# Kernel optimization log

Measured on AMD Instinct MI355X. Metric: run time of the kernel, lower is better.

Reference implementation:

```python
import jax, jax.numpy as jnp
import numpy as np

B, T, F, H = 2048, 512, 60, 7  # batch, seq_len, input_size, hidden_size


def setup_inputs() -> dict:
    key = jax.random.key(0)
    ks = jax.random.split(key, 9)
    bound = 1.0 / np.sqrt(H)  # PyTorch LSTM init: U(-1/sqrt(H), 1/sqrt(H))
    u = lambda k, s: jax.random.uniform(k, s, jnp.float32, -bound, bound)
    return {
        "x": jax.random.normal(ks[0], (B, T, F), jnp.float32),
        "Wih0": u(ks[1], (4 * H, F)),
        "Whh0": u(ks[2], (4 * H, H)),
        "bih0": u(ks[3], (4 * H,)),
        "bhh0": u(ks[4], (4 * H,)),
        "Wih1": u(ks[5], (4 * H, H)),
        "Whh1": u(ks[6], (4 * H, H)),
        "bih1": u(ks[7], (4 * H,)),
        "bhh1": u(ks[8], (4 * H,)),
    }


def _cell(xt, h, c, Wih, Whh, b):
    # PyTorch gate order: input, forget, cell(g), output
    gates = xt @ Wih.T + h @ Whh.T + b  # [B, 4H]
    i, f, g, o = jnp.split(gates, 4, axis=-1)
    c_new = jax.nn.sigmoid(f) * c + jax.nn.sigmoid(i) * jnp.tanh(g)
    h_new = jax.nn.sigmoid(o) * jnp.tanh(c_new)
    return h_new, c_new


def reference(x, Wih0, Whh0, bih0, bhh0, Wih1, Whh1, bih1, bhh1):
    b0 = bih0 + bhh0
    b1 = bih1 + bhh1
    batch = x.shape[0]
    hid = Whh0.shape[1]
    z = jnp.zeros((batch, hid), x.dtype)

    def step(carry, xt):
        h0, c0, h1, c1 = carry
        h0, c0 = _cell(xt, h0, c0, Wih0, Whh0, b0)
        h1, c1 = _cell(h0, h1, c1, Wih1, Whh1, b1)
        return (h0, c0, h1, c1), None

    xs = jnp.swapaxes(x, 0, 1)  # [T, B, F] for scan over time
    (h0, c0, h1, c1), _ = jax.lax.scan(step, (z, z, z, z), xs)
    # out[:, -1] of batch_first LSTM == final hidden state of top layer
    return h1
```

## Files before the change

kernel.cpp:

```cpp
#include <hip/hip_runtime.h>


#define B_ 2048
#define T_ 512
#define F_ 60
#define H_ 7
#define G4 28
#define BT_ (B_ * T_)
#define L2E 1.4426950408889634f
#define PD 8

#if __has_builtin(__builtin_amdgcn_exp2f)
#define EXP2(x) __builtin_amdgcn_exp2f(x)
#else
#define EXP2(x) exp2f(x)
#endif

__device__ __forceinline__ float rcpf_(float v) { return __builtin_amdgcn_rcpf(v); }

__device__ __forceinline__ float bcast(float v, int srclane) {
    return __uint_as_float(__builtin_amdgcn_readlane(__float_as_uint(v), srclane));
}

__device__ __forceinline__ float dot7(const float* w, const float* h, float seed) {
    float m01 = fmaf(w[1], h[1], w[0] * h[0]);
    float m23 = fmaf(w[3], h[3], w[2] * h[2]);
    float m45 = fmaf(w[5], h[5], w[4] * h[4]);
    float m6  = fmaf(w[6], h[6], seed);
    return (m01 + m23) + (m45 + m6);
}

__global__ __launch_bounds__(256)
void proj_kernel(const float* __restrict__ x, const float* __restrict__ Wih0,
                 const float* __restrict__ bih0, const float* __restrict__ bhh0,
                 float* __restrict__ A)
{
    __shared__ float wsm[G4 * F_];
    __shared__ float bsm[G4];

    for (int i = threadIdx.x; i < G4 * F_; i += 256) wsm[i] = Wih0[i];
    if (threadIdx.x < G4) bsm[threadIdx.x] = bih0[threadIdx.x] + bhh0[threadIdx.x];
    __syncthreads();

    const int bt = blockIdx.x * 256 + threadIdx.x;

    float xr[F_];
    const float4* __restrict__ xp = (const float4*)(x + (size_t)bt * F_);
    #pragma unroll
    for (int j = 0; j < 15; ++j) {
        float4 q = xp[j];
        xr[4 * j + 0] = q.x; xr[4 * j + 1] = q.y;
        xr[4 * j + 2] = q.z; xr[4 * j + 3] = q.w;
    }

    float4* __restrict__ Ap = (float4*)(A + (size_t)bt * G4);
    #pragma unroll
    for (int rg = 0; rg < 7; ++rg) {
        float s[4];
        #pragma unroll
        for (int q = 0; q < 4; ++q) {
            const int r = rg * 4 + q;
            const float* w = &wsm[r * F_];
            float a0 = bsm[r], a1 = 0.f, a2 = 0.f, a3 = 0.f;
            #pragma unroll
            for (int k = 0; k < F_; k += 4) {
                a0 = fmaf(w[k + 0], xr[k + 0], a0);
                a1 = fmaf(w[k + 1], xr[k + 1], a1);
                a2 = fmaf(w[k + 2], xr[k + 2], a2);
                a3 = fmaf(w[k + 3], xr[k + 3], a3);
            }
            s[q] = (a0 + a1) + (a2 + a3);
        }
        Ap[rg] = make_float4(s[0], s[1], s[2], s[3]);
    }
}

__global__ __launch_bounds__(256)
void rec_kernel(const float* __restrict__ A,
                const float* __restrict__ Whh0,
                const float* __restrict__ Wih1, const float* __restrict__ Whh1,
                const float* __restrict__ bih1, const float* __restrict__ bhh1,
                float* __restrict__ out)
{
    const int tid   = threadIdx.x;
    const int lane  = tid & 63;
    const bool isL1 = lane >= 32;
    const int g     = lane & 31;
    const int r     = (g < G4) ? g : (G4 - 1);
    const int b     = blockIdx.x * 4 + (tid >> 6);

    float wA[H_], wB[H_];
    #pragma unroll
    for (int v = 0; v < H_; ++v) {
        wA[v] = isL1 ? Wih1[r * H_ + v] : Whh0[r * H_ + v];
        wB[v] = isL1 ? Whh1[r * H_ + v] : 0.f;
    }
    const float bias1 = bih1[r] + bhh1[r];

    const bool isT = (r >= 2 * H_ && r < 3 * H_);
    const float KK = isT ? (-2.f * L2E) : (-L2E);
    const float Aa = isT ? 2.f : 1.f;
    const float Ca = isT ? -1.f : 0.f;

    float h0v[H_] = {0, 0, 0, 0, 0, 0, 0};
    float h1v[H_] = {0, 0, 0, 0, 0, 0, 0};
    float c = 0.f, hnew = 0.f;

    const float* __restrict__ pa = A + (size_t)b * T_ * G4 + r;

    float buf[PD];
    #pragma unroll
    for (int i = 0; i < PD; ++i) buf[i] = pa[i * G4];

    for (int tt = 0; tt < T_; tt += PD) {
        #pragma unroll
        for (int s = 0; s < PD; ++s) {
            const int t = tt + s;
            const int tn = (t + PD < T_) ? (t + PD) : (T_ - 1);
            float nb = pa[(size_t)tn * G4];

            float seed = isL1 ? bias1 : buf[s];
            float a = dot7(wA, h0v, seed);
            a = dot7(wB, h1v, a);
            float act = fmaf(Aa, rcpf_(1.f + EXP2(KK * a)), Ca);

            float fg = __shfl(act, lane + 7, 64);
            float gg = __shfl(act, lane + 14, 64);
            float og = __shfl(act, lane + 21, 64);

            float cnew = fmaf(fg, c, act * gg);
            if (t == 0) cnew = isL1 ? 0.f : cnew;
            c = cnew;
            float th = fmaf(2.f, rcpf_(1.f + EXP2(-2.f * L2E * c)), -1.f);
            hnew = og * th;

            #pragma unroll
            for (int v = 0; v < H_; ++v) h0v[v] = bcast(hnew, v);
            #pragma unroll
            for (int v = 0; v < H_; ++v) h1v[v] = bcast(hnew, 32 + v);

            buf[s] = nb;
        }
    }

    {
        float a = dot7(wA, h0v, isL1 ? bias1 : 0.f);
        a = dot7(wB, h1v, a);
        float act = fmaf(Aa, rcpf_(1.f + EXP2(KK * a)), Ca);
        float fg = __shfl(act, lane + 7, 64);
        float gg = __shfl(act, lane + 14, 64);
        float og = __shfl(act, lane + 21, 64);
        c = fmaf(fg, c, act * gg);
        float th = fmaf(2.f, rcpf_(1.f + EXP2(-2.f * L2E * c)), -1.f);
        hnew = og * th;
    }

    if (isL1 && g < H_) out[(size_t)b * H_ + g] = hnew;
}

#define CH 16
#define NCH (T_ / CH)
#define F4 15
#define ROW4 (CH * F4)
#define BPB 4
#define TOT4 (BPB * ROW4)

__device__ __forceinline__ float proj32(const float* pw, const float4* rp, float seed) {
    float s0 = seed, s1 = 0.f, s2 = 0.f, s3 = 0.f;
    #pragma unroll
    for (int j = 0; j < 8; ++j) {
        float4 q = rp[j];
        s0 = fmaf(pw[4 * j + 0], q.x, s0);
        s1 = fmaf(pw[4 * j + 1], q.y, s1);
        s2 = fmaf(pw[4 * j + 2], q.z, s2);
        s3 = fmaf(pw[4 * j + 3], q.w, s3);
    }
    return (s0 + s1) + (s2 + s3);
}

__global__ __launch_bounds__(256, 2)
void lstm2_fallback(const float* __restrict__ x,
                    const float* __restrict__ Wih0, const float* __restrict__ Whh0,
                    const float* __restrict__ bih0, const float* __restrict__ bhh0,
                    const float* __restrict__ Wih1, const float* __restrict__ Whh1,
                    const float* __restrict__ bih1, const float* __restrict__ bhh1,
                    float* __restrict__ out)
{
    __shared__ float4 lds4[2][BPB][ROW4];

    const int tid   = threadIdx.x;
    const int lane  = tid & 63;
    const bool isL1 = lane >= 32;
    const int g     = lane & 31;
    const int r     = (g < G4) ? g : (G4 - 1);
    const int grp   = tid >> 6;
    const int b     = blockIdx.x * BPB + grp;

    float pw[32];
    {
        const int offs = isL1 ? 28 : 0;
        #pragma unroll
        for (int k = 0; k < 32; ++k) pw[k] = Wih0[r * F_ + offs + k];
        if (isL1) { pw[0] = pw[1] = pw[2] = pw[3] = 0.f; }
    }
    float wA[H_], wB[H_];
    #pragma unroll
    for (int v = 0; v < H_; ++v) {
        wA[v] = isL1 ? Wih1[r * H_ + v] : Whh0[r * H_ + v];
        wB[v] = isL1 ? Whh1[r * H_ + v] : 0.f;
    }
    const float bias0 = bih0[r] + bhh0[r];
    const float bias1 = bih1[r] + bhh1[r];

    const bool isT = (r >= 2 * H_ && r < 3 * H_);
    const float KK = isT ? (-2.f * L2E) : (-L2E);
    const float Aa = isT ? 2.f : 1.f;
    const float Ca = isT ? -1.f : 0.f;

    float h0v[H_] = {0, 0, 0, 0, 0, 0, 0};
    float h1v[H_] = {0, 0, 0, 0, 0, 0, 0};
    float c = 0.f, hnew = 0.f;

    const float4* __restrict__ xb =
        (const float4*)(x + (size_t)(blockIdx.x * BPB) * T_ * F_);
    const int XB4 = T_ * F4;
    const int lofs = isL1 ? 7 : 0;
    const float pseed = isL1 ? 0.f : bias0;

    #pragma unroll
    for (int i = 0; i < 4; ++i) {
        int idx = tid + 256 * i;
        if (idx < TOT4) {
            int bl = idx / ROW4;
            int j  = idx - bl * ROW4;
            lds4[0][bl][j] = xb[bl * XB4 + j];
        }
    }
    __syncthreads();

    float a_in;
    {
        float ow = proj32(pw, &lds4[0][grp][0] + lofs, pseed);
        a_in = ow + __shfl(ow, lane ^ 32, 64);
    }

    for (int ch = 0; ch < NCH; ++ch) {
        const int cn = (ch < NCH - 1) ? ch + 1 : ch;
        float4 st[4];
        #pragma unroll
        for (int i = 0; i < 4; ++i) {
            int idx = tid + 256 * i;
            if (idx < TOT4) {
                int bl = idx / ROW4;
                int j  = idx - bl * ROW4;
                st[i] = xb[bl * XB4 + cn * ROW4 + j];
            }
        }

        const int buf = ch & 1;
        const float4* __restrict__ rowb = &lds4[buf][grp][0] + lofs;

        #pragma unroll
        for (int s = 0; s < CH; ++s) {
            float seed = isL1 ? bias1 : a_in;
            float a = dot7(wA, h0v, seed);
            a = dot7(wB, h1v, a);
            float act = fmaf(Aa, rcpf_(1.f + EXP2(KK * a)), Ca);

            float fg = __shfl(act, lane + 7, 64);
            float gg = __shfl(act, lane + 14, 64);
            float og = __shfl(act, lane + 21, 64);

            float cnew = fmaf(fg, c, act * gg);
            if (ch == 0 && s == 0) cnew = isL1 ? 0.f : cnew;
            c = cnew;
            float th = fmaf(2.f, rcpf_(1.f + EXP2(-2.f * L2E * c)), -1.f);
            hnew = og * th;

            #pragma unroll
            for (int v = 0; v < H_; ++v) h0v[v] = bcast(hnew, v);
            if (ch > 0 || s > 0) {
                #pragma unroll
                for (int v = 0; v < H_; ++v) h1v[v] = bcast(hnew, 32 + v);
            }

            if (s < CH - 1) {
                float ow = proj32(pw, rowb + (s + 1) * F4, pseed);
                a_in = ow + __shfl(ow, lane ^ 32, 64);
            }
        }

        #pragma unroll
        for (int i = 0; i < 4; ++i) {
            int idx = tid + 256 * i;
            if (idx < TOT4) {
                int bl = idx / ROW4;
                int j  = idx - bl * ROW4;
                lds4[buf ^ 1][bl][j] = st[i];
            }
        }
        __syncthreads();

        if (ch < NCH - 1) {
            float ow = proj32(pw, &lds4[buf ^ 1][grp][0] + lofs, pseed);
            a_in = ow + __shfl(ow, lane ^ 32, 64);
        }
    }

    {
        float a = dot7(wA, h0v, isL1 ? bias1 : 0.f);
        a = dot7(wB, h1v, a);
        float act = fmaf(Aa, rcpf_(1.f + EXP2(KK * a)), Ca);
        float fg = __shfl(act, lane + 7, 64);
        float gg = __shfl(act, lane + 14, 64);
        float og = __shfl(act, lane + 21, 64);
        c = fmaf(fg, c, act * gg);
        float th = fmaf(2.f, rcpf_(1.f + EXP2(-2.f * L2E * c)), -1.f);
        hnew = og * th;
    }

    if (isL1 && g < H_) out[(size_t)b * H_ + g] = hnew;
}

extern "C" void kernel_launch(void* const* d_in, const int* in_sizes, int n_in,
                              void* d_out, int out_size, void* d_ws, size_t ws_size,
                              hipStream_t stream) {
    const float* x    = (const float*)d_in[0];
    const float* Wih0 = (const float*)d_in[1];
    const float* Whh0 = (const float*)d_in[2];
    const float* bih0 = (const float*)d_in[3];
    const float* bhh0 = (const float*)d_in[4];
    const float* Wih1 = (const float*)d_in[5];
    const float* Whh1 = (const float*)d_in[6];
    const float* bih1 = (const float*)d_in[7];
    const float* bhh1 = (const float*)d_in[8];
    float* out = (float*)d_out;

    const size_t need = (size_t)BT_ * G4 * sizeof(float);
    if (ws_size >= need) {
        float* A = (float*)d_ws;
        proj_kernel<<<dim3(BT_ / 256), dim3(256), 0, stream>>>(x, Wih0, bih0, bhh0, A);
        rec_kernel<<<dim3(B_ / 4), dim3(256), 0, stream>>>(A, Whh0, Wih1, Whh1,
                                                           bih1, bhh1, out);
    } else {
        lstm2_fallback<<<dim3(B_ / BPB), dim3(256), 0, stream>>>(
            x, Wih0, Whh0, bih0, bhh0, Wih1, Whh1, bih1, bhh1, out);
    }
}
```

Before: 537.5 us.

## Remap input projection so each lane owns one gate row in registers

The projection kernel now keeps one gate row of Wih0 in registers per lane, and each half-wave processes one timestep row of x. The x loads are uniform across the 32 lanes of a half-wave, so they broadcast, and the output write is coalesced per row. This drops the shared-memory weight staging and the 60-element per-thread x register array. In exchange each lane recomputes nothing but loads 60 weights per thread, and 4 of every 32 lanes are idle, wasting a fraction of compute.

New measurement: 721.7 us. +34.3%, slower.

```diff
diff --git a/kernel.cpp b/kernel.cpp
--- a/kernel.cpp
+++ b/kernel.cpp
@@ -9,6 +9,7 @@
 #define BT_ (B_ * T_)
 #define L2E 1.4426950408889634f
 #define PD 8
+#define RPB 128
 
 #if __has_builtin(__builtin_amdgcn_exp2f)
 #define EXP2(x) __builtin_amdgcn_exp2f(x)
@@ -35,43 +36,38 @@
                  const float* __restrict__ bih0, const float* __restrict__ bhh0,
                  float* __restrict__ A)
 {
-    __shared__ float wsm[G4 * F_];
-    __shared__ float bsm[G4];
-
-    for (int i = threadIdx.x; i < G4 * F_; i += 256) wsm[i] = Wih0[i];
-    if (threadIdx.x < G4) bsm[threadIdx.x] = bih0[threadIdx.x] + bhh0[threadIdx.x];
-    __syncthreads();
-
-    const int bt = blockIdx.x * 256 + threadIdx.x;
-
-    float xr[F_];
-    const float4* __restrict__ xp = (const float4*)(x + (size_t)bt * F_);
-    #pragma unroll
-    for (int j = 0; j < 15; ++j) {
-        float4 q = xp[j];
-        xr[4 * j + 0] = q.x; xr[4 * j + 1] = q.y;
-        xr[4 * j + 2] = q.z; xr[4 * j + 3] = q.w;
-    }
-
-    float4* __restrict__ Ap = (float4*)(A + (size_t)bt * G4);
-    #pragma unroll
-    for (int rg = 0; rg < 7; ++rg) {
-        float s[4];
-        #pragma unroll
-        for (int q = 0; q < 4; ++q) {
-            const int r = rg * 4 + q;
-            const float* w = &wsm[r * F_];
-            float a0 = bsm[r], a1 = 0.f, a2 = 0.f, a3 = 0.f;
-            #pragma unroll
-            for (int k = 0; k < F_; k += 4) {
-                a0 = fmaf(w[k + 0], xr[k + 0], a0);
-                a1 = fmaf(w[k + 1], xr[k + 1], a1);
-                a2 = fmaf(w[k + 2], xr[k + 2], a2);
-                a3 = fmaf(w[k + 3], xr[k + 3], a3);
-            }
-            s[q] = (a0 + a1) + (a2 + a3);
-        }
-        Ap[rg] = make_float4(s[0], s[1], s[2], s[3]);
+    const int lane = threadIdx.x & 63;
+    const int wv   = threadIdx.x >> 6;
+    const int g    = lane & 31;
+    const int r    = (g < G4) ? g : (G4 - 1);
+    const int half = lane >> 5;
+
+    float wg[F_];
+    #pragma unroll
+    for (int k = 0; k < F_; ++k) wg[k] = Wih0[r * F_ + k];
+    const float bias = bih0[r] + bhh0[r];
+
+    const int row0 = blockIdx.x * RPB + wv * 32 + half;
+
+    #pragma unroll 4
+    for (int p = 0; p < 16; ++p) {
+        const int row = row0 + 2 * p;
+        const float4* __restrict__ xp = (const float4*)(x + (size_t)row * F_);
+        float4 q[15];
+        #pragma unroll
+        for (int j = 0; j < 15; ++j) q[j] = xp[j];
+
+        float s0 = bias, s1 = 0.f, s2 = 0.f, s3 = 0.f;
+        #pragma unroll
+        for (int j = 0; j < 15; ++j) {
+            s0 = fmaf(wg[4 * j + 0], q[j].x, s0);
+            s1 = fmaf(wg[4 * j + 1], q[j].y, s1);
+            s2 = fmaf(wg[4 * j + 2], q[j].z, s2);
+            s3 = fmaf(wg[4 * j + 3], q[j].w, s3);
+        }
+        float a = (s0 + s1) + (s2 + s3);
+
+        if (g < G4) A[(size_t)row * G4 + r] = a;
     }
 }
 
@@ -339,7 +335,7 @@
     const size_t need = (size_t)BT_ * G4 * sizeof(float);
     if (ws_size >= need) {
         float* A = (float*)d_ws;
-        proj_kernel<<<dim3(BT_ / 256), dim3(256), 0, stream>>>(x, Wih0, bih0, bhh0, A);
+        proj_kernel<<<dim3(BT_ / RPB), dim3(256), 0, stream>>>(x, Wih0, bih0, bhh0, A);
         rec_kernel<<<dim3(B_ / 4), dim3(256), 0, stream>>>(A, Whh0, Wih1, Whh1,
                                                            bih1, bhh1, out);
     } else {
```

## Interleave gate layout for DPP quad broadcasts and register-tile input projection

Applied to the files above, without the earlier changes.

The input projection kernel now has each thread compute four rows, with weights read as float4 from shared memory and the next x chunk prefetched. Each weight load is then reused across four rows. The A buffer is written in a gate-interleaved order (i,f,g,o adjacent per hidden unit). This lets the recurrent kernel gather gates with DPP quad_perm moves instead of ds_bpermute shuffles, shortening the serial per-step critical path. The recurrent prefetch is restructured into a block load of the next 8 steps. The trade-offs are higher register pressure in the projection kernel (112 accumulators) and more complex indexing.

After: 668.5 us. 24.4% more time.

```diff
diff --git a/kernel.cpp b/kernel.cpp
--- a/kernel.cpp
+++ b/kernel.cpp
@@ -9,12 +9,17 @@
 #define BT_ (B_ * T_)
 #define L2E 1.4426950408889634f
 #define PD 8
+#define RPT 4
+#define PRB (256 * RPT)
 
 #if __has_builtin(__builtin_amdgcn_exp2f)
 #define EXP2(x) __builtin_amdgcn_exp2f(x)
 #else
 #define EXP2(x) exp2f(x)
 #endif
+
+#define QUADB(v, pat) \
+    __int_as_float(__builtin_amdgcn_mov_dpp(__float_as_int(v), pat, 0xF, 0xF, true))
 
 __device__ __forceinline__ float rcpf_(float v) { return __builtin_amdgcn_rcpf(v); }
 
@@ -35,43 +40,63 @@
                  const float* __restrict__ bih0, const float* __restrict__ bhh0,
                  float* __restrict__ A)
 {
-    __shared__ float wsm[G4 * F_];
-    __shared__ float bsm[G4];
-
-    for (int i = threadIdx.x; i < G4 * F_; i += 256) wsm[i] = Wih0[i];
-    if (threadIdx.x < G4) bsm[threadIdx.x] = bih0[threadIdx.x] + bhh0[threadIdx.x];
+    __shared__ float4 wsm4[G4 * 15];
+    __shared__ float  bsm[G4];
+
+    const int tid = threadIdx.x;
+    for (int i = tid; i < G4 * 15; i += 256) wsm4[i] = ((const float4*)Wih0)[i];
+    if (tid < G4) bsm[tid] = bih0[tid] + bhh0[tid];
     __syncthreads();
 
-    const int bt = blockIdx.x * 256 + threadIdx.x;
-
-    float xr[F_];
-    const float4* __restrict__ xp = (const float4*)(x + (size_t)bt * F_);
-    #pragma unroll
+    const int row0 = blockIdx.x * PRB + tid;
+
+    float acc[G4][RPT];
+    #pragma unroll
+    for (int p = 0; p < G4; ++p) {
+        const int r = (p & 3) * 7 + (p >> 2);
+        const float bb = bsm[r];
+        #pragma unroll
+        for (int rr = 0; rr < RPT; ++rr) acc[p][rr] = bb;
+    }
+
+    const float* bp[RPT];
+    #pragma unroll
+    for (int rr = 0; rr < RPT; ++rr) bp[rr] = x + (size_t)(row0 + 256 * rr) * F_;
+
+    float4 qc[RPT], qn[RPT];
+    #pragma unroll
+    for (int rr = 0; rr < RPT; ++rr) qc[rr] = *(const float4*)(bp[rr]);
+
+    #pragma unroll 1
     for (int j = 0; j < 15; ++j) {
-        float4 q = xp[j];
-        xr[4 * j + 0] = q.x; xr[4 * j + 1] = q.y;
-        xr[4 * j + 2] = q.z; xr[4 * j + 3] = q.w;
-    }
-
-    float4* __restrict__ Ap = (float4*)(A + (size_t)bt * G4);
-    #pragma unroll
-    for (int rg = 0; rg < 7; ++rg) {
-        float s[4];
-        #pragma unroll
-        for (int q = 0; q < 4; ++q) {
-            const int r = rg * 4 + q;
-            const float* w = &wsm[r * F_];
-            float a0 = bsm[r], a1 = 0.f, a2 = 0.f, a3 = 0.f;
-            #pragma unroll
-            for (int k = 0; k < F_; k += 4) {
-                a0 = fmaf(w[k + 0], xr[k + 0], a0);
-                a1 = fmaf(w[k + 1], xr[k + 1], a1);
-                a2 = fmaf(w[k + 2], xr[k + 2], a2);
-                a3 = fmaf(w[k + 3], xr[k + 3], a3);
-            }
-            s[q] = (a0 + a1) + (a2 + a3);
-        }
-        Ap[rg] = make_float4(s[0], s[1], s[2], s[3]);
+        const int jn = (j < 14) ? j + 1 : 14;
+        #pragma unroll
+        for (int rr = 0; rr < RPT; ++rr)
+            qn[rr] = *(const float4*)(bp[rr] + 4 * jn);
+
+        #pragma unroll
+        for (int p = 0; p < G4; ++p) {
+            const int r = (p & 3) * 7 + (p >> 2);
+            float4 w = wsm4[r * 15 + j];
+            #pragma unroll
+            for (int rr = 0; rr < RPT; ++rr) {
+                acc[p][rr] = fmaf(w.x, qc[rr].x, acc[p][rr]);
+                acc[p][rr] = fmaf(w.y, qc[rr].y, acc[p][rr]);
+                acc[p][rr] = fmaf(w.z, qc[rr].z, acc[p][rr]);
+                acc[p][rr] = fmaf(w.w, qc[rr].w, acc[p][rr]);
+            }
+        }
+        #pragma unroll
+        for (int rr = 0; rr < RPT; ++rr) qc[rr] = qn[rr];
+    }
+
+    #pragma unroll
+    for (int rr = 0; rr < RPT; ++rr) {
+        float4* __restrict__ Ap = (float4*)(A + (size_t)(row0 + 256 * rr) * G4);
+        #pragma unroll
+        for (int u = 0; u < 7; ++u)
+            Ap[u] = make_float4(acc[4 * u + 0][rr], acc[4 * u + 1][rr],
+                                acc[4 * u + 2][rr], acc[4 * u + 3][rr]);
     }
 }
 
@@ -82,12 +107,15 @@
                 const float* __restrict__ bih1, const float* __restrict__ bhh1,
                 float* __restrict__ out)
 {
-    const int tid   = threadIdx.x;
-    const int lane  = tid & 63;
+    const int tid  = threadIdx.x;
+    const int lane = tid & 63;
     const bool isL1 = lane >= 32;
-    const int g     = lane & 31;
-    const int r     = (g < G4) ? g : (G4 - 1);
-    const int b     = blockIdx.x * 4 + (tid >> 6);
+    const int l5 = lane & 31;
+    const int gi = lane & 3;
+    const int u  = l5 >> 2;
+    const int r  = min(gi * 7 + u, G4 - 1);
+    const int pos = min(l5, G4 - 1);
+    const int b  = blockIdx.x * 4 + (tid >> 6);
 
     float wA[H_], wB[H_];
     #pragma unroll
@@ -97,7 +125,7 @@
     }
     const float bias1 = bih1[r] + bhh1[r];
 
-    const bool isT = (r >= 2 * H_ && r < 3 * H_);
+    const bool isT = (gi == 2);
     const float KK = isT ? (-2.f * L2E) : (-L2E);
     const float Aa = isT ? 2.f : 1.f;
     const float Ca = isT ? -1.f : 0.f;
@@ -106,40 +134,45 @@
     float h1v[H_] = {0, 0, 0, 0, 0, 0, 0};
     float c = 0.f, hnew = 0.f;
 
-    const float* __restrict__ pa = A + (size_t)b * T_ * G4 + r;
-
-    float buf[PD];
-    #pragma unroll
-    for (int i = 0; i < PD; ++i) buf[i] = pa[i * G4];
-
+    const float* __restrict__ pa = A + (size_t)b * T_ * G4 + pos;
+
+    float buf[PD], nxt[PD];
+    #pragma unroll
+    for (int i = 0; i < PD; ++i) buf[i] = pa[(size_t)i * G4];
+
+    #pragma unroll 1
     for (int tt = 0; tt < T_; tt += PD) {
+        const bool more = (tt + PD < T_);
+        if (more) {
+            #pragma unroll
+            for (int i = 0; i < PD; ++i) nxt[i] = pa[(size_t)(tt + PD + i) * G4];
+        }
         #pragma unroll
         for (int s = 0; s < PD; ++s) {
-            const int t = tt + s;
-            const int tn = (t + PD < T_) ? (t + PD) : (T_ - 1);
-            float nb = pa[(size_t)tn * G4];
-
             float seed = isL1 ? bias1 : buf[s];
             float a = dot7(wA, h0v, seed);
             a = dot7(wB, h1v, a);
             float act = fmaf(Aa, rcpf_(1.f + EXP2(KK * a)), Ca);
 
-            float fg = __shfl(act, lane + 7, 64);
-            float gg = __shfl(act, lane + 14, 64);
-            float og = __shfl(act, lane + 21, 64);
-
-            float cnew = fmaf(fg, c, act * gg);
-            if (t == 0) cnew = isL1 ? 0.f : cnew;
+            float vi = QUADB(act, 0x00);
+            float vf = QUADB(act, 0x55);
+            float vg = QUADB(act, 0xAA);
+            float vo = QUADB(act, 0xFF);
+
+            float cnew = fmaf(vf, c, vi * vg);
+            if (tt == 0 && s == 0) cnew = isL1 ? 0.f : cnew;
             c = cnew;
             float th = fmaf(2.f, rcpf_(1.f + EXP2(-2.f * L2E * c)), -1.f);
-            hnew = og * th;
-
-            #pragma unroll
-            for (int v = 0; v < H_; ++v) h0v[v] = bcast(hnew, v);
-            #pragma unroll
-            for (int v = 0; v < H_; ++v) h1v[v] = bcast(hnew, 32 + v);
-
-            buf[s] = nb;
+            hnew = vo * th;
+
+            #pragma unroll
+            for (int v = 0; v < H_; ++v) h0v[v] = bcast(hnew, 4 * v);
+            #pragma unroll
+            for (int v = 0; v < H_; ++v) h1v[v] = bcast(hnew, 32 + 4 * v);
+        }
+        if (more) {
+            #pragma unroll
+            for (int i = 0; i < PD; ++i) buf[i] = nxt[i];
         }
     }
 
@@ -147,15 +180,16 @@
         float a = dot7(wA, h0v, isL1 ? bias1 : 0.f);
         a = dot7(wB, h1v, a);
         float act = fmaf(Aa, rcpf_(1.f + EXP2(KK * a)), Ca);
-        float fg = __shfl(act, lane + 7, 64);
-        float gg = __shfl(act, lane + 14, 64);
-        float og = __shfl(act, lane + 21, 64);
-        c = fmaf(fg, c, act * gg);
+        float vi = QUADB(act, 0x00);
+        float vf = QUADB(act, 0x55);
+        float vg = QUADB(act, 0xAA);
+        float vo = QUADB(act, 0xFF);
+        c = fmaf(vf, c, vi * vg);
         float th = fmaf(2.f, rcpf_(1.f + EXP2(-2.f * L2E * c)), -1.f);
-        hnew = og * th;
-    }
-
-    if (isL1 && g < H_) out[(size_t)b * H_ + g] = hnew;
+        hnew = vo * th;
+    }
+
+    if (isL1 && gi == 0 && u < H_) out[(size_t)b * H_ + u] = hnew;
 }
 
 #define CH 16
@@ -339,7 +373,7 @@
     const size_t need = (size_t)BT_ * G4 * sizeof(float);
     if (ws_size >= need) {
         float* A = (float*)d_ws;
-        proj_kernel<<<dim3(BT_ / 256), dim3(256), 0, stream>>>(x, Wih0, bih0, bhh0, A);
+        proj_kernel<<<dim3(BT_ / PRB), dim3(256), 0, stream>>>(x, Wih0, bih0, bhh0, A);
         rec_kernel<<<dim3(B_ / 4), dim3(256), 0, stream>>>(A, Whh0, Wih1, Whh1,
                                                            bih1, bhh1, out);
     } else {
```
